# Optimization experiments

Measured on AMD Instinct MI355X. Metric: run time of the kernel, lower is better.

The kernel has to match this reference:

```python
import jax, jax.numpy as jnp
import numpy as np

N_NODES = 100000
N_EDGES = 1600000
D_IN = 128
D_OUT = 5


def setup_inputs() -> dict:
    key = jax.random.key(0)
    k1, k2, k3, k4, k5 = jax.random.split(key, 5)
    x = jax.random.normal(k1, (N_NODES, D_IN), dtype=jnp.float32)
    edge_index = jax.random.randint(k2, (2, N_EDGES), 0, N_NODES, dtype=jnp.int64)
    scale = 1.0 / np.sqrt(D_IN)
    W_l = jax.random.normal(k3, (D_OUT, D_IN), dtype=jnp.float32) * scale
    b_l = jax.random.normal(k4, (D_OUT,), dtype=jnp.float32) * scale
    W_r = jax.random.normal(k5, (D_OUT, D_IN), dtype=jnp.float32) * scale
    return {"x": x, "edge_index": edge_index, "W_l": W_l, "b_l": b_l, "W_r": W_r}


def reference(x, edge_index, W_l, b_l, W_r):
    # PyG SAGEConv with aggr='mean', root_weight=True:
    # out_i = mean_{j: (j->i) in E} x_j @ W_l^T + b_l + x_i @ W_r^T
    n = x.shape[0]
    src = edge_index[0]
    dst = edge_index[1]
    msgs = x[src]  # [E, D_in] gather (irregular access)
    agg_sum = jax.ops.segment_sum(msgs, dst, num_segments=n)  # [N, D_in]
    deg = jax.ops.segment_sum(jnp.ones(src.shape, dtype=x.dtype), dst, num_segments=n)
    agg_mean = agg_sum / jnp.maximum(deg, 1.0)[:, None]  # zero-degree nodes -> 0
    out = agg_mean @ W_l.T + b_l + x @ W_r.T  # [N, D_out]
    return out
```

## Files before the change

### kernel.cpp

```cpp
#include <hip/hip_runtime.h>
#include <hip/hip_fp16.h>


#define N_NODES 100000
#define N_EDGES 1600000
#define D_IN 128

#define HR_STRIDE 8
#define N_PAD 100352

#define B_NODES 196
#define N_BUCKETS 512
#define CAP 3840

#define SC_EPT 16
#define SC_EPB (256 * SC_EPT)
#define SC_GRID ((N_EDGES + SC_EPB - 1) / SC_EPB)

#define PROJ_NPB 128
#define PROJ_BLOCKS ((N_NODES + PROJ_NPB - 1) / PROJ_NPB)
#define FUSED_GRID (PROJ_BLOCKS + SC_GRID)

#define BB 32
#define NBATCH (PROJ_NPB / BB)
#define XB_BYTES (BB * 512)

#define FXS 262144.0f
#define FXB 16777216u
#define FXBF 16777216.0f
#define INV_FXS (1.0f / 262144.0f)

typedef unsigned long long u64;
typedef unsigned int u32;

__device__ __forceinline__ float dot8(const float4 a0, const float4 a1,
                                      const float4 b0, const float4 b1) {
    return a0.x * b0.x + a0.y * b0.y + a0.z * b0.z + a0.w * b0.w
         + a1.x * b1.x + a1.y * b1.y + a1.z * b1.z + a1.w * b1.w;
}

__global__ __launch_bounds__(256, 4) void proj_scatter_kernel(
    const float* __restrict__ x,
    const float* __restrict__ Wl,
    const float* __restrict__ Wr,
    uint4* __restrict__ hl,
    float* __restrict__ hr,
    const int* __restrict__ ei,
    u32* __restrict__ sorted,
    int* __restrict__ cursor)
{
    const int tid = threadIdx.x;
    const int m   = blockIdx.x % 3;
    const int d   = blockIdx.x / 3;

    if (m < 2) {
        __shared__ __align__(16) char xbuf[2][XB_BYTES];

        const int pidx = d * 2 + m;
        const int g = tid >> 4;
        const int k = tid & 15;
        const int node0blk = pidx * PROJ_NPB;

        const char* xb = (const char*)x;
        const size_t XLIM = (size_t)N_NODES * 512 - 16;

        float4 wv[10][2];
#pragma unroll
        for (int o = 0; o < 10; ++o) {
            const float* w = (o < 5 ? Wl + o * D_IN : Wr + (o - 5) * D_IN) + k * 8;
            wv[o][0] = ((const float4*)w)[0];
            wv[o][1] = ((const float4*)w)[1];
        }

#define STAGE(bufi, batch)                                                   \
        {                                                                    \
            const size_t gb0 = (size_t)(node0blk + (batch) * BB) * 512;      \
            _Pragma("unroll")                                                \
            for (int r = 0; r < 4; ++r) {                                    \
                const int loff = r * 4096 + tid * 16;                        \
                size_t goff = gb0 + (size_t)loff;                            \
                goff = goff > XLIM ? XLIM : goff;                            \
                __builtin_amdgcn_global_load_lds(                            \
                    (const __attribute__((address_space(1))) void*)(xb + goff), \
                    (__attribute__((address_space(3))) void*)(&xbuf[bufi][loff]), \
                    16, 0, 0);                                               \
            }                                                                \
        }

        int cur = 0;
        STAGE(0, 0);

#pragma unroll
        for (int b = 0; b < NBATCH; ++b) {
            if (b + 1 < NBATCH) {
                STAGE(cur ^ 1, b + 1);
                asm volatile("s_waitcnt vmcnt(4)" ::: "memory");
            } else {
                asm volatile("s_waitcnt vmcnt(0)" ::: "memory");
            }
            __builtin_amdgcn_s_barrier();
            asm volatile("" ::: "memory");

            const char* xbc = (const char*)xbuf[cur];
#pragma unroll
            for (int u = 0; u < 2; ++u) {
                const int nlb  = g * 2 + u;
                const int node = node0blk + b * BB + nlb;
                const float4* xp = (const float4*)(xbc + nlb * 512 + k * 32);
                float4 x0 = xp[0];
                float4 x1 = xp[1];

                float s[10];
#pragma unroll
                for (int o = 0; o < 10; ++o)
                    s[o] = dot8(x0, x1, wv[o][0], wv[o][1]);

#pragma unroll
                for (int o = 0; o < 10; ++o) {
                    s[o] += __shfl_xor(s[o], 8, 64);
                    s[o] += __shfl_xor(s[o], 4, 64);
                    s[o] += __shfl_xor(s[o], 2, 64);
                    s[o] += __shfl_xor(s[o], 1, 64);
                }

                if (k == 0) {
                    u32 u0 = (u32)__half_as_ushort(__float2half_rn(s[0]));
                    u32 u1 = (u32)__half_as_ushort(__float2half_rn(s[1]));
                    u32 u2 = (u32)__half_as_ushort(__float2half_rn(s[2]));
                    u32 u3 = (u32)__half_as_ushort(__float2half_rn(s[3]));
                    u32 u4 = (u32)__half_as_ushort(__float2half_rn(s[4]));
                    uint4 pk;
                    pk.x = u0 | (u1 << 16);
                    pk.y = u2 | (u3 << 16);
                    pk.z = u4;
                    pk.w = 0u;
                    hl[node] = pk;

                    float* pr = hr + (size_t)node * HR_STRIDE;
                    *(float4*)pr = make_float4(s[5], s[6], s[7], s[8]);
                    pr[4] = s[9];
                }
            }
            __builtin_amdgcn_s_barrier();
            asm volatile("" ::: "memory");
            cur ^= 1;
        }
#undef STAGE
    } else {
        __shared__ int hist[N_BUCKETS];
        __shared__ int basepos[N_BUCKETS];

        for (int i = tid; i < N_BUCKETS; i += 256) hist[i] = 0;
        __syncthreads();

        const int e0 = d * SC_EPB + tid * SC_EPT;

        int srcv[SC_EPT], dstv[SC_EPT], slot[SC_EPT];
        bool valid[SC_EPT];

        if (e0 + SC_EPT <= N_EDGES) {
            const int4* s4 = (const int4*)(ei + e0);
            const int4* d4 = (const int4*)(ei + N_EDGES + e0);
#pragma unroll
            for (int c = 0; c < SC_EPT / 4; ++c) {
                int4 sv = s4[c], dv = d4[c];
                srcv[c*4+0] = sv.x; srcv[c*4+1] = sv.y;
                srcv[c*4+2] = sv.z; srcv[c*4+3] = sv.w;
                dstv[c*4+0] = dv.x; dstv[c*4+1] = dv.y;
                dstv[c*4+2] = dv.z; dstv[c*4+3] = dv.w;
            }
#pragma unroll
            for (int q = 0; q < SC_EPT; ++q) valid[q] = true;
        } else {
#pragma unroll
            for (int q = 0; q < SC_EPT; ++q) {
                int e = e0 + q;
                valid[q] = (e < N_EDGES);
                srcv[q] = valid[q] ? ei[e] : 0;
                dstv[q] = valid[q] ? ei[N_EDGES + e] : 0;
            }
        }

#pragma unroll
        for (int q = 0; q < SC_EPT; ++q) {
            if (valid[q]) {
                unsigned b = (unsigned)dstv[q] / 196u;
                slot[q] = atomicAdd(&hist[b], 1);
            }
        }
        __syncthreads();

        for (int b = tid; b < N_BUCKETS; b += 256) {
            int c = hist[b];
            if (c > 0) basepos[b] = atomicAdd(&cursor[b], c);
        }
        __syncthreads();

#pragma unroll
        for (int q = 0; q < SC_EPT; ++q) {
            if (valid[q]) {
                unsigned b = (unsigned)dstv[q] / 196u;
                unsigned r = (unsigned)dstv[q] - b * 196u;
                sorted[(size_t)b * CAP + basepos[b] + slot[q]] =
                    (r << 17) | (unsigned)srcv[q];
            }
        }
    }
}

__global__ __launch_bounds__(512) void agg_kernel(
    const u32* __restrict__ sorted,
    const int* __restrict__ cursor,
    const uint4* __restrict__ hl,
    const float* __restrict__ hr,
    const float* __restrict__ bias,
    float* __restrict__ out)
{
    __shared__ u64 acc[B_NODES * 3];

    const int b   = blockIdx.x;
    const int tid = threadIdx.x;

    for (int i = tid; i < B_NODES * 3; i += 512) acc[i] = 0ull;
    __syncthreads();

    const int cnt = cursor[b];
    const u32* sp = sorted + (size_t)b * CAP;
    const int nvec = cnt >> 2;

#define EMITH(hv, rr)                                                        \
    {                                                                        \
        float g0 = __half2float(__ushort_as_half((unsigned short)((hv).x & 0xFFFFu))); \
        float g1 = __half2float(__ushort_as_half((unsigned short)((hv).x >> 16)));     \
        float g2 = __half2float(__ushort_as_half((unsigned short)((hv).y & 0xFFFFu))); \
        float g3 = __half2float(__ushort_as_half((unsigned short)((hv).y >> 16)));     \
        float g4 = __half2float(__ushort_as_half((unsigned short)((hv).z & 0xFFFFu))); \
        u32 f0 = __float2uint_rn(fmaf(g0, FXS, FXBF));                       \
        u32 f1 = __float2uint_rn(fmaf(g1, FXS, FXBF));                       \
        u32 f2 = __float2uint_rn(fmaf(g2, FXS, FXBF));                       \
        u32 f3 = __float2uint_rn(fmaf(g3, FXS, FXBF));                       \
        u32 f4 = __float2uint_rn(fmaf(g4, FXS, FXBF));                       \
        u64* a = acc + (rr) * 3;                                             \
        atomicAdd(&a[0], ((u64)f1 << 32) | f0);                              \
        atomicAdd(&a[1], ((u64)f3 << 32) | f2);                              \
        atomicAdd(&a[2], ((u64)f4 << 32) | 1u);                              \
    }

    for (int it = tid; it < nvec; it += 512) {
        uint4 v = ((const uint4*)sp)[it];
        int s0 = (int)(v.x & 0x1FFFFu), r0 = (int)(v.x >> 17);
        int s1 = (int)(v.y & 0x1FFFFu), r1 = (int)(v.y >> 17);
        int s2 = (int)(v.z & 0x1FFFFu), r2 = (int)(v.z >> 17);
        int s3 = (int)(v.w & 0x1FFFFu), r3 = (int)(v.w >> 17);

        uint4 a0 = hl[s0];
        uint4 a1 = hl[s1];
        uint4 a2 = hl[s2];
        uint4 a3 = hl[s3];

        EMITH(a0, r0) EMITH(a1, r1) EMITH(a2, r2) EMITH(a3, r3)
    }
    for (int i = (nvec << 2) + tid; i < cnt; i += 512) {
        u32 v = sp[i];
        int src = (int)(v & 0x1FFFFu);
        int r   = (int)(v >> 17);
        uint4 a = hl[src];
        EMITH(a, r)
    }
#undef EMITH
    __syncthreads();

    const int nodebase = b * B_NODES;
    for (int n = tid; n < B_NODES; n += 512) {
        int node = nodebase + n;
        if (node >= N_NODES) continue;
        u64 w0 = acc[n * 3 + 0];
        u64 w1 = acc[n * 3 + 1];
        u64 w2 = acc[n * 3 + 2];
        u32 deg = (u32)(w2 & 0xFFFFFFFFu);
        u32 db  = deg * FXB;
        int i0 = (int)((u32)(w0 & 0xFFFFFFFFu) - db);
        int i1 = (int)((u32)(w0 >> 32)         - db);
        int i2 = (int)((u32)(w1 & 0xFFFFFFFFu) - db);
        int i3 = (int)((u32)(w1 >> 32)         - db);
        int i4 = (int)((u32)(w2 >> 32)         - db);

        float rec = INV_FXS / fmaxf((float)deg, 1.0f);
        const float* h = hr + (size_t)node * HR_STRIDE;
        float* o = out + (size_t)node * 5;
        o[0] = (float)i0 * rec + bias[0] + h[0];
        o[1] = (float)i1 * rec + bias[1] + h[1];
        o[2] = (float)i2 * rec + bias[2] + h[2];
        o[3] = (float)i3 * rec + bias[3] + h[3];
        o[4] = (float)i4 * rec + bias[4] + h[4];
    }
}

extern "C" void kernel_launch(void* const* d_in, const int* in_sizes, int n_in,
                              void* d_out, int out_size, void* d_ws, size_t ws_size,
                              hipStream_t stream) {
    const float* x    = (const float*)d_in[0];
    const int*   ei   = (const int*)d_in[1];
    const float* Wl   = (const float*)d_in[2];
    const float* bl   = (const float*)d_in[3];
    const float* Wr   = (const float*)d_in[4];
    float*       out  = (float*)d_out;

    uint4* hl     = (uint4*)d_ws;
    float* hr     = (float*)(hl + N_PAD);
    u32*   sorted = (u32*)(hr + (size_t)N_PAD * HR_STRIDE);
    int*   cursor = (int*)(sorted + (size_t)N_BUCKETS * CAP);

    hipMemsetAsync(cursor, 0, N_BUCKETS * sizeof(int), stream);

    proj_scatter_kernel<<<FUSED_GRID, 256, 0, stream>>>(
        x, Wl, Wr, hl, hr, ei, sorted, cursor);

    agg_kernel<<<N_BUCKETS, 512, 0, stream>>>(sorted, cursor, hl, hr, bl, out);
}
```

Measured before the change: 128.6 us.

## Split fused proj/scatter kernel and replace atomic aggregation with LDS counting sort

Splits the fused projection/scatter kernel into two separate launches and restructures projection so each wave double-buffers its own x tile without block barriers. Scatter uses 8 edges per thread. The aggregation kernel now counting-sorts each bucket's edges by destination in shared memory and sums fp16 projections per node serially with two threads per node, replacing 64-bit fixed-point shared atomics. This removes atomic contention but adds an extra launch, loses proj/scatter overlap, and introduces serial gather latency chains per node.

Result: slower. 153.7 us (+19.5%).

```diff
diff --git a/kernel.cpp b/kernel.cpp
--- a/kernel.cpp
+++ b/kernel.cpp
@@ -13,22 +13,12 @@
 #define N_BUCKETS 512
 #define CAP 3840
 
-#define SC_EPT 16
+#define SC_EPT 8
 #define SC_EPB (256 * SC_EPT)
 #define SC_GRID ((N_EDGES + SC_EPB - 1) / SC_EPB)
 
 #define PROJ_NPB 128
 #define PROJ_BLOCKS ((N_NODES + PROJ_NPB - 1) / PROJ_NPB)
-#define FUSED_GRID (PROJ_BLOCKS + SC_GRID)
-
-#define BB 32
-#define NBATCH (PROJ_NPB / BB)
-#define XB_BYTES (BB * 512)
-
-#define FXS 262144.0f
-#define FXB 16777216u
-#define FXBF 16777216.0f
-#define INV_FXS (1.0f / 262144.0f)
 
 typedef unsigned long long u64;
 typedef unsigned int u32;
@@ -39,174 +29,171 @@
          + a1.x * b1.x + a1.y * b1.y + a1.z * b1.z + a1.w * b1.w;
 }
 
-__global__ __launch_bounds__(256, 4) void proj_scatter_kernel(
+__global__ __launch_bounds__(256, 4) void proj_kernel(
     const float* __restrict__ x,
     const float* __restrict__ Wl,
     const float* __restrict__ Wr,
     uint4* __restrict__ hl,
-    float* __restrict__ hr,
+    float* __restrict__ hr)
+{
+    __shared__ __align__(16) char xb[4][2][4096];
+
+    const int tid  = threadIdx.x;
+    const int wvi  = tid >> 6;
+    const int lane = tid & 63;
+    const int g    = lane >> 4;
+    const int k    = lane & 15;
+
+    const int wnode0 = blockIdx.x * PROJ_NPB + wvi * 32;
+    const char* xbytes = (const char*)x;
+    const size_t XLIM = (size_t)N_NODES * 512 - 16;
+
+    float4 wv[10][2];
+#pragma unroll
+    for (int o = 0; o < 10; ++o) {
+        const float* w = (o < 5 ? Wl + o * D_IN : Wr + (o - 5) * D_IN) + k * 8;
+        wv[o][0] = ((const float4*)w)[0];
+        wv[o][1] = ((const float4*)w)[1];
+    }
+
+#define PSTAGE(bufi, batch)                                                  \
+    {                                                                        \
+        const size_t gb0 = (size_t)(wnode0 + (batch) * 8) * 512;             \
+        _Pragma("unroll")                                                    \
+        for (int r = 0; r < 4; ++r) {                                        \
+            const int loff = r * 1024 + lane * 16;                           \
+            size_t goff = gb0 + (size_t)loff;                                \
+            goff = goff > XLIM ? XLIM : goff;                                \
+            __builtin_amdgcn_global_load_lds(                                \
+                (const __attribute__((address_space(1))) void*)(xbytes + goff), \
+                (__attribute__((address_space(3))) void*)(&xb[wvi][bufi][loff]), \
+                16, 0, 0);                                                   \
+        }                                                                    \
+    }
+
+    PSTAGE(0, 0);
+    PSTAGE(1, 1);
+
+#pragma unroll
+    for (int b = 0; b < 4; ++b) {
+        if (b == 3) asm volatile("s_waitcnt vmcnt(0)" ::: "memory");
+        else        asm volatile("s_waitcnt vmcnt(4)" ::: "memory");
+
+        const char* xc = &xb[wvi][b & 1][0];
+#pragma unroll
+        for (int u = 0; u < 2; ++u) {
+            const int nlb  = g * 2 + u;
+            const int node = wnode0 + b * 8 + nlb;
+            const float4* xp = (const float4*)(xc + nlb * 512 + k * 32);
+            float4 x0 = xp[0];
+            float4 x1 = xp[1];
+
+            float s[10];
+#pragma unroll
+            for (int o = 0; o < 10; ++o)
+                s[o] = dot8(x0, x1, wv[o][0], wv[o][1]);
+
+#pragma unroll
+            for (int o = 0; o < 10; ++o) {
+                s[o] += __shfl_xor(s[o], 8, 64);
+                s[o] += __shfl_xor(s[o], 4, 64);
+                s[o] += __shfl_xor(s[o], 2, 64);
+                s[o] += __shfl_xor(s[o], 1, 64);
+            }
+
+            if (k == 0) {
+                u32 u0 = (u32)__half_as_ushort(__float2half_rn(s[0]));
+                u32 u1 = (u32)__half_as_ushort(__float2half_rn(s[1]));
+                u32 u2 = (u32)__half_as_ushort(__float2half_rn(s[2]));
+                u32 u3 = (u32)__half_as_ushort(__float2half_rn(s[3]));
+                u32 u4 = (u32)__half_as_ushort(__float2half_rn(s[4]));
+                uint4 pk;
+                pk.x = u0 | (u1 << 16);
+                pk.y = u2 | (u3 << 16);
+                pk.z = u4;
+                pk.w = 0u;
+                hl[node] = pk;
+
+                float* pr = hr + (size_t)node * HR_STRIDE;
+                *(float4*)pr = make_float4(s[5], s[6], s[7], s[8]);
+                pr[4] = s[9];
+            }
+        }
+        if (b < 2) {
+            asm volatile("s_waitcnt lgkmcnt(0)" ::: "memory");
+            PSTAGE(b & 1, b + 2);
+        }
+    }
+#undef PSTAGE
+}
+
+__global__ __launch_bounds__(256) void scatter_kernel(
     const int* __restrict__ ei,
     u32* __restrict__ sorted,
     int* __restrict__ cursor)
 {
+    __shared__ int hist[N_BUCKETS];
+    __shared__ int basepos[N_BUCKETS];
+
     const int tid = threadIdx.x;
-    const int m   = blockIdx.x % 3;
-    const int d   = blockIdx.x / 3;
-
-    if (m < 2) {
-        __shared__ __align__(16) char xbuf[2][XB_BYTES];
-
-        const int pidx = d * 2 + m;
-        const int g = tid >> 4;
-        const int k = tid & 15;
-        const int node0blk = pidx * PROJ_NPB;
-
-        const char* xb = (const char*)x;
-        const size_t XLIM = (size_t)N_NODES * 512 - 16;
-
-        float4 wv[10][2];
-#pragma unroll
-        for (int o = 0; o < 10; ++o) {
-            const float* w = (o < 5 ? Wl + o * D_IN : Wr + (o - 5) * D_IN) + k * 8;
-            wv[o][0] = ((const float4*)w)[0];
-            wv[o][1] = ((const float4*)w)[1];
-        }
-
-#define STAGE(bufi, batch)                                                   \
-        {                                                                    \
-            const size_t gb0 = (size_t)(node0blk + (batch) * BB) * 512;      \
-            _Pragma("unroll")                                                \
-            for (int r = 0; r < 4; ++r) {                                    \
-                const int loff = r * 4096 + tid * 16;                        \
-                size_t goff = gb0 + (size_t)loff;                            \
-                goff = goff > XLIM ? XLIM : goff;                            \
-                __builtin_amdgcn_global_load_lds(                            \
-                    (const __attribute__((address_space(1))) void*)(xb + goff), \
-                    (__attribute__((address_space(3))) void*)(&xbuf[bufi][loff]), \
-                    16, 0, 0);                                               \
-            }                                                                \
-        }
-
-        int cur = 0;
-        STAGE(0, 0);
-
-#pragma unroll
-        for (int b = 0; b < NBATCH; ++b) {
-            if (b + 1 < NBATCH) {
-                STAGE(cur ^ 1, b + 1);
-                asm volatile("s_waitcnt vmcnt(4)" ::: "memory");
-            } else {
-                asm volatile("s_waitcnt vmcnt(0)" ::: "memory");
-            }
-            __builtin_amdgcn_s_barrier();
-            asm volatile("" ::: "memory");
-
-            const char* xbc = (const char*)xbuf[cur];
-#pragma unroll
-            for (int u = 0; u < 2; ++u) {
-                const int nlb  = g * 2 + u;
-                const int node = node0blk + b * BB + nlb;
-                const float4* xp = (const float4*)(xbc + nlb * 512 + k * 32);
-                float4 x0 = xp[0];
-                float4 x1 = xp[1];
-
-                float s[10];
-#pragma unroll
-                for (int o = 0; o < 10; ++o)
-                    s[o] = dot8(x0, x1, wv[o][0], wv[o][1]);
-
-#pragma unroll
-                for (int o = 0; o < 10; ++o) {
-                    s[o] += __shfl_xor(s[o], 8, 64);
-                    s[o] += __shfl_xor(s[o], 4, 64);
-                    s[o] += __shfl_xor(s[o], 2, 64);
-                    s[o] += __shfl_xor(s[o], 1, 64);
-                }
-
-                if (k == 0) {
-                    u32 u0 = (u32)__half_as_ushort(__float2half_rn(s[0]));
-                    u32 u1 = (u32)__half_as_ushort(__float2half_rn(s[1]));
-                    u32 u2 = (u32)__half_as_ushort(__float2half_rn(s[2]));
-                    u32 u3 = (u32)__half_as_ushort(__float2half_rn(s[3]));
-                    u32 u4 = (u32)__half_as_ushort(__float2half_rn(s[4]));
-                    uint4 pk;
-                    pk.x = u0 | (u1 << 16);
-                    pk.y = u2 | (u3 << 16);
-                    pk.z = u4;
-                    pk.w = 0u;
-                    hl[node] = pk;
-
-                    float* pr = hr + (size_t)node * HR_STRIDE;
-                    *(float4*)pr = make_float4(s[5], s[6], s[7], s[8]);
-                    pr[4] = s[9];
-                }
-            }
-            __builtin_amdgcn_s_barrier();
-            asm volatile("" ::: "memory");
-            cur ^= 1;
-        }
-#undef STAGE
+    for (int i = tid; i < N_BUCKETS; i += 256) hist[i] = 0;
+    __syncthreads();
+
+    const int e0 = blockIdx.x * SC_EPB + tid * SC_EPT;
+
+    int srcv[SC_EPT], dstv[SC_EPT], slot[SC_EPT];
+    bool valid[SC_EPT];
+
+    if (e0 + SC_EPT <= N_EDGES) {
+        const int4* s4 = (const int4*)(ei + e0);
+        const int4* d4 = (const int4*)(ei + N_EDGES + e0);
+#pragma unroll
+        for (int c = 0; c < SC_EPT / 4; ++c) {
+            int4 sv = s4[c], dv = d4[c];
+            srcv[c*4+0] = sv.x; srcv[c*4+1] = sv.y;
+            srcv[c*4+2] = sv.z; srcv[c*4+3] = sv.w;
+            dstv[c*4+0] = dv.x; dstv[c*4+1] = dv.y;
+            dstv[c*4+2] = dv.z; dstv[c*4+3] = dv.w;
+        }
+#pragma unroll
+        for (int q = 0; q < SC_EPT; ++q) valid[q] = true;
     } else {
-        __shared__ int hist[N_BUCKETS];
-        __shared__ int basepos[N_BUCKETS];
-
-        for (int i = tid; i < N_BUCKETS; i += 256) hist[i] = 0;
-        __syncthreads();
-
-        const int e0 = d * SC_EPB + tid * SC_EPT;
-
-        int srcv[SC_EPT], dstv[SC_EPT], slot[SC_EPT];
-        bool valid[SC_EPT];
-
-        if (e0 + SC_EPT <= N_EDGES) {
-            const int4* s4 = (const int4*)(ei + e0);
-            const int4* d4 = (const int4*)(ei + N_EDGES + e0);
-#pragma unroll
-            for (int c = 0; c < SC_EPT / 4; ++c) {
-                int4 sv = s4[c], dv = d4[c];
-                srcv[c*4+0] = sv.x; srcv[c*4+1] = sv.y;
-                srcv[c*4+2] = sv.z; srcv[c*4+3] = sv.w;
-                dstv[c*4+0] = dv.x; dstv[c*4+1] = dv.y;
-                dstv[c*4+2] = dv.z; dstv[c*4+3] = dv.w;
-            }
-#pragma unroll
-            for (int q = 0; q < SC_EPT; ++q) valid[q] = true;
-        } else {
-#pragma unroll
-            for (int q = 0; q < SC_EPT; ++q) {
-                int e = e0 + q;
-                valid[q] = (e < N_EDGES);
-                srcv[q] = valid[q] ? ei[e] : 0;
-                dstv[q] = valid[q] ? ei[N_EDGES + e] : 0;
-            }
-        }
-
 #pragma unroll
         for (int q = 0; q < SC_EPT; ++q) {
-            if (valid[q]) {
-                unsigned b = (unsigned)dstv[q] / 196u;
-                slot[q] = atomicAdd(&hist[b], 1);
-            }
-        }
-        __syncthreads();
-
-        for (int b = tid; b < N_BUCKETS; b += 256) {
-            int c = hist[b];
-            if (c > 0) basepos[b] = atomicAdd(&cursor[b], c);
-        }
-        __syncthreads();
-
-#pragma unroll
-        for (int q = 0; q < SC_EPT; ++q) {
-            if (valid[q]) {
-                unsigned b = (unsigned)dstv[q] / 196u;
-                unsigned r = (unsigned)dstv[q] - b * 196u;
-                sorted[(size_t)b * CAP + basepos[b] + slot[q]] =
-                    (r << 17) | (unsigned)srcv[q];
-            }
-        }
-    }
-}
+            int e = e0 + q;
+            valid[q] = (e < N_EDGES);
+            srcv[q] = valid[q] ? ei[e] : 0;
+            dstv[q] = valid[q] ? ei[N_EDGES + e] : 0;
+        }
+    }
+
+#pragma unroll
+    for (int q = 0; q < SC_EPT; ++q) {
+        if (valid[q]) {
+            unsigned b = (unsigned)dstv[q] / 196u;
+            slot[q] = atomicAdd(&hist[b], 1);
+        }
+    }
+    __syncthreads();
+
+    for (int b = tid; b < N_BUCKETS; b += 256) {
+        int c = hist[b];
+        if (c > 0) basepos[b] = atomicAdd(&cursor[b], c);
+    }
+    __syncthreads();
+
+#pragma unroll
+    for (int q = 0; q < SC_EPT; ++q) {
+        if (valid[q]) {
+            unsigned b = (unsigned)dstv[q] / 196u;
+            unsigned r = (unsigned)dstv[q] - b * 196u;
+            sorted[(size_t)b * CAP + basepos[b] + slot[q]] =
+                (r << 17) | (unsigned)srcv[q];
+        }
+    }
+}
+
+#define AGG_T 512
 
 __global__ __launch_bounds__(512) void agg_kernel(
     const u32* __restrict__ sorted,
@@ -216,83 +203,96 @@
     const float* __restrict__ bias,
     float* __restrict__ out)
 {
-    __shared__ u64 acc[B_NODES * 3];
+    __shared__ u32 hist[B_NODES];
+    __shared__ u32 deg[B_NODES];
+    __shared__ u32 offs[B_NODES];
+    __shared__ u32 srcs[CAP];
+    __shared__ float part[B_NODES][5];
 
     const int b   = blockIdx.x;
     const int tid = threadIdx.x;
 
-    for (int i = tid; i < B_NODES * 3; i += 512) acc[i] = 0ull;
-    __syncthreads();
-
-    const int cnt = cursor[b];
+    for (int i = tid; i < B_NODES; i += AGG_T) hist[i] = 0u;
+    __syncthreads();
+
+    const int cnt = min(cursor[b], CAP);
     const u32* sp = sorted + (size_t)b * CAP;
-    const int nvec = cnt >> 2;
-
-#define EMITH(hv, rr)                                                        \
-    {                                                                        \
-        float g0 = __half2float(__ushort_as_half((unsigned short)((hv).x & 0xFFFFu))); \
-        float g1 = __half2float(__ushort_as_half((unsigned short)((hv).x >> 16)));     \
-        float g2 = __half2float(__ushort_as_half((unsigned short)((hv).y & 0xFFFFu))); \
-        float g3 = __half2float(__ushort_as_half((unsigned short)((hv).y >> 16)));     \
-        float g4 = __half2float(__ushort_as_half((unsigned short)((hv).z & 0xFFFFu))); \
-        u32 f0 = __float2uint_rn(fmaf(g0, FXS, FXBF));                       \
-        u32 f1 = __float2uint_rn(fmaf(g1, FXS, FXBF));                       \
-        u32 f2 = __float2uint_rn(fmaf(g2, FXS, FXBF));                       \
-        u32 f3 = __float2uint_rn(fmaf(g3, FXS, FXBF));                       \
-        u32 f4 = __float2uint_rn(fmaf(g4, FXS, FXBF));                       \
-        u64* a = acc + (rr) * 3;                                             \
-        atomicAdd(&a[0], ((u64)f1 << 32) | f0);                              \
-        atomicAdd(&a[1], ((u64)f3 << 32) | f2);                              \
-        atomicAdd(&a[2], ((u64)f4 << 32) | 1u);                              \
-    }
-
-    for (int it = tid; it < nvec; it += 512) {
-        uint4 v = ((const uint4*)sp)[it];
-        int s0 = (int)(v.x & 0x1FFFFu), r0 = (int)(v.x >> 17);
-        int s1 = (int)(v.y & 0x1FFFFu), r1 = (int)(v.y >> 17);
-        int s2 = (int)(v.z & 0x1FFFFu), r2 = (int)(v.z >> 17);
-        int s3 = (int)(v.w & 0x1FFFFu), r3 = (int)(v.w >> 17);
-
-        uint4 a0 = hl[s0];
-        uint4 a1 = hl[s1];
-        uint4 a2 = hl[s2];
-        uint4 a3 = hl[s3];
-
-        EMITH(a0, r0) EMITH(a1, r1) EMITH(a2, r2) EMITH(a3, r3)
-    }
-    for (int i = (nvec << 2) + tid; i < cnt; i += 512) {
-        u32 v = sp[i];
-        int src = (int)(v & 0x1FFFFu);
-        int r   = (int)(v >> 17);
-        uint4 a = hl[src];
-        EMITH(a, r)
-    }
-#undef EMITH
-    __syncthreads();
-
-    const int nodebase = b * B_NODES;
-    for (int n = tid; n < B_NODES; n += 512) {
-        int node = nodebase + n;
-        if (node >= N_NODES) continue;
-        u64 w0 = acc[n * 3 + 0];
-        u64 w1 = acc[n * 3 + 1];
-        u64 w2 = acc[n * 3 + 2];
-        u32 deg = (u32)(w2 & 0xFFFFFFFFu);
-        u32 db  = deg * FXB;
-        int i0 = (int)((u32)(w0 & 0xFFFFFFFFu) - db);
-        int i1 = (int)((u32)(w0 >> 32)         - db);
-        int i2 = (int)((u32)(w1 & 0xFFFFFFFFu) - db);
-        int i3 = (int)((u32)(w1 >> 32)         - db);
-        int i4 = (int)((u32)(w2 >> 32)         - db);
-
-        float rec = INV_FXS / fmaxf((float)deg, 1.0f);
-        const float* h = hr + (size_t)node * HR_STRIDE;
-        float* o = out + (size_t)node * 5;
-        o[0] = (float)i0 * rec + bias[0] + h[0];
-        o[1] = (float)i1 * rec + bias[1] + h[1];
-        o[2] = (float)i2 * rec + bias[2] + h[2];
-        o[3] = (float)i3 * rec + bias[3] + h[3];
-        o[4] = (float)i4 * rec + bias[4] + h[4];
+
+    u32 ev[8];
+    int rv[8], sl[8];
+#pragma unroll
+    for (int q = 0; q < 8; ++q) {
+        int i = tid + q * AGG_T;
+        ev[q] = (i < cnt) ? sp[i] : 0xFFFFFFFFu;
+    }
+#pragma unroll
+    for (int q = 0; q < 8; ++q) {
+        if (ev[q] != 0xFFFFFFFFu) {
+            rv[q] = (int)(ev[q] >> 17);
+            sl[q] = (int)atomicAdd(&hist[rv[q]], 1u);
+        }
+    }
+    __syncthreads();
+
+    if (tid < B_NODES) { deg[tid] = hist[tid]; offs[tid] = hist[tid]; }
+    __syncthreads();
+#pragma unroll
+    for (int s = 1; s < B_NODES; s <<= 1) {
+        u32 v = 0;
+        if (tid < B_NODES && tid >= s) v = offs[tid - s];
+        __syncthreads();
+        if (tid < B_NODES) offs[tid] += v;
+        __syncthreads();
+    }
+    if (tid < B_NODES) offs[tid] -= deg[tid];
+    __syncthreads();
+
+#pragma unroll
+    for (int q = 0; q < 8; ++q) {
+        if (ev[q] != 0xFFFFFFFFu)
+            srcs[offs[rv[q]] + (u32)sl[q]] = ev[q] & 0x1FFFFu;
+    }
+    __syncthreads();
+
+    float a0 = 0.f, a1 = 0.f, a2 = 0.f, a3 = 0.f, a4 = 0.f;
+    if (tid < 2 * B_NODES) {
+        const int p = (tid >= B_NODES);
+        const int n = p ? tid - B_NODES : tid;
+        const u32 d = deg[n];
+        const u32 o = offs[n];
+        const u32 h0 = (d + 1) >> 1;
+        const u32 i0 = p ? o + h0 : o;
+        const u32 i1 = p ? o + d : o + h0;
+        for (u32 i = i0; i < i1; ++i) {
+            u32 s = srcs[i];
+            uint4 h = hl[s];
+            a0 += __half2float(__ushort_as_half((unsigned short)(h.x & 0xFFFFu)));
+            a1 += __half2float(__ushort_as_half((unsigned short)(h.x >> 16)));
+            a2 += __half2float(__ushort_as_half((unsigned short)(h.y & 0xFFFFu)));
+            a3 += __half2float(__ushort_as_half((unsigned short)(h.y >> 16)));
+            a4 += __half2float(__ushort_as_half((unsigned short)(h.z & 0xFFFFu)));
+        }
+        if (p) {
+            part[n][0] = a0; part[n][1] = a1; part[n][2] = a2;
+            part[n][3] = a3; part[n][4] = a4;
+        }
+    }
+    __syncthreads();
+
+    if (tid < B_NODES) {
+        const int node = b * B_NODES + tid;
+        if (node < N_NODES) {
+            a0 += part[tid][0]; a1 += part[tid][1]; a2 += part[tid][2];
+            a3 += part[tid][3]; a4 += part[tid][4];
+            const float rec = 1.0f / fmaxf((float)deg[tid], 1.0f);
+            const float* h = hr + (size_t)node * HR_STRIDE;
+            float* o = out + (size_t)node * 5;
+            o[0] = a0 * rec + bias[0] + h[0];
+            o[1] = a1 * rec + bias[1] + h[1];
+            o[2] = a2 * rec + bias[2] + h[2];
+            o[3] = a3 * rec + bias[3] + h[3];
+            o[4] = a4 * rec + bias[4] + h[4];
+        }
     }
 }
 
@@ -313,8 +313,7 @@
 
     hipMemsetAsync(cursor, 0, N_BUCKETS * sizeof(int), stream);
 
-    proj_scatter_kernel<<<FUSED_GRID, 256, 0, stream>>>(
-        x, Wl, Wr, hl, hr, ei, sorted, cursor);
-
+    proj_kernel<<<PROJ_BLOCKS, 256, 0, stream>>>(x, Wl, Wr, hl, hr);
+    scatter_kernel<<<SC_GRID, 256, 0, stream>>>(ei, sorted, cursor);
     agg_kernel<<<N_BUCKETS, 512, 0, stream>>>(sorted, cursor, hl, hr, bl, out);
 }
```
